# Kernel tuning notes

Measured on AMD Instinct MI355X. Metric: run time of the kernel, lower is better.

Reference implementation:

```python
import jax, jax.numpy as jnp
import numpy as np

B, K, S, H, V, T = 32, 5, 64, 768, 30522, 40
SEP = 102


def setup_inputs() -> dict:
    key = jax.random.key(0)
    ks = jax.random.split(key, 8)
    s = 0.02
    return {
        "src": jax.random.normal(ks[0], (B, S, H), jnp.float32),
        "E": jax.random.normal(ks[1], (V, H), jnp.float32) * s,
        "Wa": jax.random.normal(ks[2], (H, H), jnp.float32) * s,
        "Ua": jax.random.normal(ks[3], (H, H), jnp.float32) * s,
        "va": jax.random.normal(ks[4], (H,), jnp.float32) * s,
        "W_ih": jax.random.normal(ks[5], (3 * H, 2 * H), jnp.float32) * s,
        "W_hh": jax.random.normal(ks[6], (3 * H, H), jnp.float32) * s,
        "b_ih": jnp.zeros((3 * H,), jnp.float32),
        "b_hh": jnp.zeros((3 * H,), jnp.float32),
        "Wo": jax.random.normal(ks[7], (V, H), jnp.float32) * s,
        "bo": jnp.zeros((V,), jnp.float32),
    }


def _decoder(tok, src, h, E, Wa, Ua, va, W_ih, W_hh, b_ih, b_hh, Wo, bo):
    # tok [N] int, src [N,S,H], h [N,H] -> (logits [N,V], h_new [N,H])
    emb = E[tok]                                              # [N,H]
    e = jnp.tanh(src @ Wa + (h @ Ua)[:, None, :]) @ va        # [N,S]
    a = jax.nn.softmax(e, axis=-1)
    ctx = jnp.einsum('ns,nsd->nd', a, src)                    # [N,H]
    x = jnp.concatenate([emb, ctx], axis=-1)                  # [N,2H]
    gx = x @ W_ih.T + b_ih
    gh = h @ W_hh.T + b_hh
    xr, xz, xn = jnp.split(gx, 3, axis=-1)
    hr, hz, hn = jnp.split(gh, 3, axis=-1)
    r = jax.nn.sigmoid(xr + hr)
    z = jax.nn.sigmoid(xz + hz)
    n = jnp.tanh(xn + r * hn)
    h2 = (1.0 - z) * n + z * h
    return h2 @ Wo.T + bo, h2


def _search(src, E, Wa, Ua, va, W_ih, W_hh, b_ih, b_hh, Wo, bo):
    P = (E, Wa, Ua, va, W_ih, W_hh, b_ih, b_hh, Wo, bo)
    # step 0: start token 102, zero hidden
    tok0 = jnp.full((B,), SEP, jnp.int32)
    logits, h = _decoder(tok0, src, jnp.zeros((B, H), src.dtype), *P)
    logp = jax.nn.log_softmax(logits, axis=-1)
    scores, toks = jax.lax.top_k(logp, K)                     # [B,K]
    hiddens = jnp.broadcast_to(h[:, None, :], (B, K, H))
    src_k = jnp.broadcast_to(src[:, None], (B, K, S, H)).reshape(B * K, S, H)
    no_prob = jnp.full((V,), -1e9, src.dtype).at[SEP].set(0.0)
    beam_mask = jnp.arange(K) < K - 1  # original normalizes only first k-1 segments

    def body(carry, _):
        toks, maps, hiddens, scores, ended, lengths = carry
        # parent hidden per beam (gather by backpointer), decode all beams at once
        h_in = jnp.take_along_axis(hiddens, maps[:, :, None], axis=1)  # [B,K,H]
        logits, h_new = _decoder(toks.reshape(-1), src_k, h_in.reshape(B * K, H), *P)
        logp = jax.nn.log_softmax(logits, axis=-1).reshape(B, K, V)
        logp = jnp.where(ended[:, :, None] == 0, logp, no_prob)
        lengths = lengths + (ended == 0).astype(lengths.dtype)
        cand = logp + scores[:, :, None]                      # [B,K,V]
        denom = jnp.where(beam_mask, lengths ** 0.7, 1.0)     # [B,K]
        norm = (cand / denom[:, :, None]).reshape(B, K * V)
        _, idx = jax.lax.top_k(norm, K)                       # [B,K]
        new_scores = jnp.take_along_axis(cand.reshape(B, K * V), idx, axis=1)
        new_toks = (idx % V).astype(jnp.int32)
        new_maps = (idx // V).astype(jnp.int32)
        ended = jnp.where(new_toks == SEP, 1.0, ended)
        new_carry = (new_toks, new_maps, h_new.reshape(B, K, H), new_scores, ended, lengths)
        return new_carry, (new_toks, new_maps)

    carry0 = (toks.astype(jnp.int32), jnp.zeros((B, K), jnp.int32), hiddens,
              scores, jnp.zeros((B, K), src.dtype), jnp.zeros((B, K), src.dtype))
    carryF, (toks_seq, maps_seq) = jax.lax.scan(body, carry0, None, length=T - 1)
    toks_all = jnp.concatenate([toks[None].astype(jnp.int32), toks_seq], axis=0)   # [T,B,K]
    maps_all = jnp.concatenate([jnp.zeros((1, B, K), jnp.int32), maps_seq], axis=0)
    final_scores = carryF[3]
    best = jnp.argmax(final_scores, axis=1).astype(jnp.int32)  # [B]

    def back(idx, tm):
        tk, mp = tm
        out = jnp.take_along_axis(tk, idx[:, None], axis=1)[:, 0]
        nxt = jnp.take_along_axis(mp, idx[:, None], axis=1)[:, 0]
        return nxt, out

    _, outs = jax.lax.scan(back, best, (toks_all, maps_all), reverse=True)
    return outs.T, final_scores  # tokens [B,T], scores [B,K]


def reference(src, E, Wa, Ua, va, W_ih, W_hh, b_ih, b_hh, Wo, bo):
    tokens, _ = _search(src, E, Wa, Ua, va, W_ih, W_hh, b_ih, b_hh, Wo, bo)
    return tokens
```

## Files before the change

### kernel.cpp

```cpp
#include <hip/hip_runtime.h>
#include <cmath>

#define Hdim 768
#define Bb 32
#define Kb 5
#define Ss 64
#define Vv 30522
#define Tt 40
#define SEPTOK 102
#define NTLOG 477

typedef __attribute__((ext_vector_type(2))) float f32x2;
typedef __attribute__((ext_vector_type(4))) float f32x4;

struct Params {
    const float *src, *E, *Wa, *Ua, *va, *W_ih, *W_hh, *b_ih, *b_hh, *Wo, *bo;
    float *srcWa, *hA, *hB, *hUa, *gxE, *gh;
    float *mt_g; double *st_g; float *t5v; int *t5j;
    float *scores, *ended, *lengths;
    int *toks_cur, *maps_cur, *toks_all, *maps_all, *outTok;
};

__device__ __forceinline__ bool betterf(float va, int ja, float vb, int jb) {
    return (va > vb) || (va == vb && ja < jb);
}
__device__ __forceinline__ void ins5(float* tv, int* tj, float v, int j) {
    if (!betterf(v, j, tv[4], tj[4])) return;
    tv[4] = v; tj[4] = j;
#pragma unroll
    for (int q = 4; q > 0; q--) {
        if (betterf(tv[q], tj[q], tv[q - 1], tj[q - 1])) {
            float t = tv[q]; tv[q] = tv[q - 1]; tv[q - 1] = t;
            int  ti = tj[q]; tj[q] = tj[q - 1]; tj[q - 1] = ti;
        }
    }
}
__device__ __forceinline__ void ins5p(float* tv, int* tj, float* tx,
                                      float v, int j, float x) {
    if (!betterf(v, j, tv[4], tj[4])) return;
    tv[4] = v; tj[4] = j; tx[4] = x;
#pragma unroll
    for (int q = 4; q > 0; q--) {
        if (betterf(tv[q], tj[q], tv[q - 1], tj[q - 1])) {
            float t = tv[q]; tv[q] = tv[q - 1]; tv[q - 1] = t;
            int  ti = tj[q]; tj[q] = tj[q - 1]; tj[q - 1] = ti;
            float tz = tx[q]; tx[q] = tx[q - 1]; tx[q - 1] = tz;
        }
    }
}

struct GS { float xs[32][162]; float wt[32][68]; };

__device__ void gemm512(GS& sm, const Params& P, int t, int N, int xsrc,
    int i0, int Pdim, const float* __restrict__ W, int ldW, bool pmaj,
    const float* __restrict__ bias, float* __restrict__ outp, int ldO, int Icap)
{
    const int tid = threadIdx.x;
    const int ty = tid >> 5, tx = tid & 31;
    const float* h_old = (t & 1) ? P.hB : P.hA;

    float acc[10][2];
#pragma unroll
    for (int j = 0; j < 10; j++) { acc[j][0] = 0.f; acc[j][1] = 0.f; }

    for (int c0 = 0; c0 < Pdim; c0 += 32) {
        __syncthreads();
        for (int e = tid; e < 160 * 32; e += 512) {
            int r = e >> 5, p = e & 31;
            int n = (r < N) ? r : (N - 1);
            float v = 0.f;
            if (xsrc == 0) {
                if (t != 0) {
                    int par = (n / Kb) * Kb + P.maps_cur[n];
                    v = h_old[(size_t)par * Hdim + c0 + p];
                }
            } else {
                int tok = (t == 0) ? SEPTOK : P.toks_cur[n];
                v = P.E[(size_t)tok * Hdim + c0 + p];
            }
            sm.xs[p][r] = v;
        }
        if (pmaj) {
            int p = tid >> 4, i4 = (tid & 15) * 4;
            int gi = i0 + i4;
            f32x4 a;
            if (gi + 3 < Icap) {
                a = *(const f32x4*)&W[(size_t)(c0 + p) * ldW + gi];
            } else {
#pragma unroll
                for (int u = 0; u < 4; u++) {
                    int g = gi + u; if (g >= Icap) g = Icap - 1;
                    a[u] = W[(size_t)(c0 + p) * ldW + g];
                }
            }
            *(f32x4*)&sm.wt[p][i4] = a;
        } else {
            int c = tid >> 3, p4 = (tid & 7) * 4;
            int gi = i0 + c; if (gi >= Icap) gi = Icap - 1;
            f32x4 a = *(const f32x4*)&W[(size_t)gi * ldW + c0 + p4];
            sm.wt[p4 + 0][c] = a[0]; sm.wt[p4 + 1][c] = a[1];
            sm.wt[p4 + 2][c] = a[2]; sm.wt[p4 + 3][c] = a[3];
        }
        __syncthreads();
        float part[10][2];
#pragma unroll
        for (int j = 0; j < 10; j++) { part[j][0] = 0.f; part[j][1] = 0.f; }
#pragma unroll
        for (int p = 0; p < 32; p++) {
            f32x2 w2 = *(const f32x2*)&sm.wt[p][tx * 2];
            float xr[10];
#pragma unroll
            for (int j = 0; j < 10; j += 2) {
                f32x2 xv = *(const f32x2*)&sm.xs[p][ty * 10 + j];
                xr[j] = xv.x; xr[j + 1] = xv.y;
            }
#pragma unroll
            for (int j = 0; j < 10; j++) {
                part[j][0] = fmaf(xr[j], w2.x, part[j][0]);
                part[j][1] = fmaf(xr[j], w2.y, part[j][1]);
            }
        }
#pragma unroll
        for (int j = 0; j < 10; j++) {
            acc[j][0] = __fadd_rn(acc[j][0], part[j][0]);
            acc[j][1] = __fadd_rn(acc[j][1], part[j][1]);
        }
    }
#pragma unroll
    for (int j = 0; j < 10; j++) {
        int r = ty * 10 + j;
        if (r < N) {
#pragma unroll
            for (int u = 0; u < 2; u++) {
                int gi = i0 + tx * 2 + u;
                if (gi < Icap) {
                    float v = acc[j][u];
                    if (bias) v = __fadd_rn(v, bias[gi]);
                    outp[(size_t)r * ldO + gi] = v;
                }
            }
        }
    }
}

__global__ __launch_bounds__(512) void p1_k(Params P, int t, int N)
{
    __shared__ GS sm;
    int task = blockIdx.x;
    if (task < 12)
        gemm512(sm, P, t, N, 0, task * 64, Hdim, P.Ua, Hdim, true,
                nullptr, P.hUa, Hdim, Hdim);
    else if (task < 48)
        gemm512(sm, P, t, N, 0, (task - 12) * 64, Hdim, P.W_hh, Hdim, false,
                P.b_hh, P.gh, 2304, 2304);
    else
        gemm512(sm, P, t, N, 1, (task - 48) * 64, Hdim, P.W_ih, 1536, false,
                nullptr, P.gxE, 2304, 2304);
}

__global__ __launch_bounds__(512) void p2_k(Params P, int t, int N)
{
    __shared__ float hu[Hdim];
    __shared__ float va_s[Hdim];
    __shared__ float e_s[Ss];
    __shared__ float a_s[Ss];
    __shared__ float ctx[Hdim];
    __shared__ float gx[2304];
    const int tid = threadIdx.x;
    const int n = blockIdx.x;
    if (n >= N) return;
    const int Kcur = (t == 0) ? 1 : Kb;
    const int b = n / Kcur;
    float* h_new = (t & 1) ? P.hA : P.hB;
    const float* h_old = (t & 1) ? P.hB : P.hA;

    for (int j = tid; j < Hdim; j += 512) {
        hu[j]   = P.hUa[(size_t)n * Hdim + j];
        va_s[j] = P.va[j];
    }
    __syncthreads();
    {
        int wv = tid >> 6, ln = tid & 63;
        for (int s = wv * 8; s < wv * 8 + 8; s++) {
            const float* sw = P.srcWa + (size_t)(b * Ss + s) * Hdim;
            double p = 0.0;
            for (int j = ln; j < Hdim; j += 64) {
                float tv = tanhf(__fadd_rn(sw[j], hu[j]));
                p = ::fma((double)tv, (double)va_s[j], p);
            }
            for (int off = 32; off; off >>= 1) p += __shfl_down(p, off, 64);
            if (ln == 0) e_s[s] = (float)p;
        }
    }
    __syncthreads();
    if (tid < 64) {
        float v = e_s[tid], m = v;
        for (int off = 32; off; off >>= 1) m = fmaxf(m, __shfl_xor(m, off, 64));
        float p = expf(__fsub_rn(v, m));
        double sum = (double)p;
        for (int off = 32; off; off >>= 1) sum += __shfl_xor(sum, off, 64);
        a_s[tid] = __fdiv_rn(p, (float)sum);
    }
    __syncthreads();
    for (int j = tid; j < Hdim; j += 512) {
        double acc = 0.0;
        for (int s = 0; s < Ss; s++)
            acc = ::fma((double)a_s[s],
                        (double)P.src[(size_t)(b * Ss + s) * Hdim + j], acc);
        ctx[j] = (float)acc;
    }
    __syncthreads();
    for (int i = tid; i < 2304; i += 512) {
        const float* wr = P.W_ih + (size_t)i * 1536 + 768;
        float accv = 0.f, part = 0.f;
        for (int p = 0; p < 768; p += 4) {
            f32x4 w4 = *(const f32x4*)&wr[p];
            part = fmaf(ctx[p + 0], w4[0], part);
            part = fmaf(ctx[p + 1], w4[1], part);
            part = fmaf(ctx[p + 2], w4[2], part);
            part = fmaf(ctx[p + 3], w4[3], part);
            if ((p & 31) == 28) { accv = __fadd_rn(accv, part); part = 0.f; }
        }
        gx[i] = __fadd_rn(__fadd_rn(P.gxE[(size_t)n * 2304 + i], accv), P.b_ih[i]);
    }
    __syncthreads();
    int par = 0;
    if (t != 0) par = (n / Kb) * Kb + P.maps_cur[n];
    for (int i = tid; i < Hdim; i += 512) {
        float xr = gx[i], xz = gx[768 + i], xn = gx[1536 + i];
        const float* ghr = P.gh + (size_t)n * 2304;
        float hr = ghr[i], hz = ghr[768 + i], hn = ghr[1536 + i];
        float r  = __fdiv_rn(1.f, __fadd_rn(1.f, expf(-__fadd_rn(xr, hr))));
        float z  = __fdiv_rn(1.f, __fadd_rn(1.f, expf(-__fadd_rn(xz, hz))));
        float nn = tanhf(__fadd_rn(xn, __fmul_rn(r, hn)));
        float hv = (t == 0) ? 0.f : h_old[(size_t)par * Hdim + i];
        float h2 = __fadd_rn(__fmul_rn(__fsub_rn(1.f, z), nn), __fmul_rn(z, hv));
        if (t == 0) {
            for (int k = 0; k < Kb; k++)
                h_new[(size_t)(n * Kb + k) * Hdim + i] = h2;
        } else {
            h_new[(size_t)n * Hdim + i] = h2;
        }
    }
}

__global__ __launch_bounds__(512) void p4_k(Params P, int t, int N)
{
    __shared__ GS sm;
    const int tid = threadIdx.x;
    const int ty = tid >> 5, tx = tid & 31;
    const int task = blockIdx.x;
    const int i0 = task * 64;
    const float* h_new = (t & 1) ? P.hA : P.hB;
    const int rowMul = (t == 0) ? Kb : 1;

    float acc[10][2];
#pragma unroll
    for (int j = 0; j < 10; j++) { acc[j][0] = 0.f; acc[j][1] = 0.f; }

    for (int c0 = 0; c0 < Hdim; c0 += 32) {
        __syncthreads();
        for (int e = tid; e < 160 * 32; e += 512) {
            int r = e >> 5, p = e & 31;
            int n = (r < N) ? r : (N - 1);
            sm.xs[p][r] = h_new[((size_t)n * rowMul) * Hdim + c0 + p];
        }
        {
            int c = tid >> 3, p4 = (tid & 7) * 4;
            int gi = i0 + c; if (gi >= Vv) gi = Vv - 1;
            f32x4 a = *(const f32x4*)&P.Wo[(size_t)gi * Hdim + c0 + p4];
            sm.wt[p4 + 0][c] = a[0]; sm.wt[p4 + 1][c] = a[1];
            sm.wt[p4 + 2][c] = a[2]; sm.wt[p4 + 3][c] = a[3];
        }
        __syncthreads();
        float part[10][2];
#pragma unroll
        for (int j = 0; j < 10; j++) { part[j][0] = 0.f; part[j][1] = 0.f; }
#pragma unroll
        for (int p = 0; p < 32; p++) {
            f32x2 w2 = *(const f32x2*)&sm.wt[p][tx * 2];
            float xr[10];
#pragma unroll
            for (int j = 0; j < 10; j += 2) {
                f32x2 xv = *(const f32x2*)&sm.xs[p][ty * 10 + j];
                xr[j] = xv.x; xr[j + 1] = xv.y;
            }
#pragma unroll
            for (int j = 0; j < 10; j++) {
                part[j][0] = fmaf(xr[j], w2.x, part[j][0]);
                part[j][1] = fmaf(xr[j], w2.y, part[j][1]);
            }
        }
#pragma unroll
        for (int j = 0; j < 10; j++) {
            acc[j][0] = __fadd_rn(acc[j][0], part[j][0]);
            acc[j][1] = __fadd_rn(acc[j][1], part[j][1]);
        }
    }
#pragma unroll
    for (int j = 0; j < 10; j++) {
        int r = ty * 10 + j;
        int g0 = i0 + tx * 2, g1 = g0 + 1;
        float x0 = (g0 < Vv) ? __fadd_rn(acc[j][0], P.bo[g0]) : -INFINITY;
        float x1 = (g1 < Vv) ? __fadd_rn(acc[j][1], P.bo[g1]) : -INFINITY;
        float mr = fmaxf(x0, x1);
#pragma unroll
        for (int off = 16; off; off >>= 1)
            mr = fmaxf(mr, __shfl_xor(mr, off, 32));
        double s = (double)expf(__fsub_rn(x0, mr)) + (double)expf(__fsub_rn(x1, mr));
#pragma unroll
        for (int off = 16; off; off >>= 1)
            s += __shfl_xor(s, off, 32);
        float tv[5]; int tj[5];
#pragma unroll
        for (int q = 0; q < 5; q++) { tv[q] = -INFINITY; tj[q] = 0x7fffffff; }
        ins5(tv, tj, x0, (g0 < Vv) ? g0 : 0x7fffffff);
        ins5(tv, tj, x1, (g1 < Vv) ? g1 : 0x7fffffff);
#pragma unroll
        for (int lv = 1; lv < 32; lv <<= 1) {
            float pv[5]; int pj[5];
#pragma unroll
            for (int q = 0; q < 5; q++) {
                pv[q] = __shfl_xor(tv[q], lv, 32);
                pj[q] = __shfl_xor(tj[q], lv, 32);
            }
#pragma unroll
            for (int q = 0; q < 5; q++) ins5(tv, tj, pv[q], pj[q]);
        }
        if (tx == 0 && r < N) {
            P.mt_g[(size_t)task * 160 + r] = mr;
            P.st_g[(size_t)task * 160 + r] = s;
#pragma unroll
            for (int q = 0; q < 5; q++) {
                P.t5v[((size_t)task * 160 + r) * 5 + q] = tv[q];
                P.t5j[((size_t)task * 160 + r) * 5 + q] = tj[q];
            }
        }
    }
}

__global__ __launch_bounds__(512) void p5_k(Params P, int t)
{
    __shared__ float sc[Kb], den[Kb], endd[Kb], len[Kb], mxs[Kb], lgv[Kb];
    __shared__ float mv[256 * 5]; __shared__ int mj[256 * 5];
    __shared__ float mxp[256 * 5];
    __shared__ float rv[512]; __shared__ int rj[512]; __shared__ float rx[512];
    __shared__ double rd[512];
    __shared__ int selj[Kb]; __shared__ float selx[Kb];
    const int tid = threadIdx.x;
    const int b = blockIdx.x;
    const int Kcur = (t == 0) ? 1 : Kb;

    if (tid < Kb) {
        if (t == 0) {
            sc[tid] = 0.f; endd[tid] = 0.f; len[tid] = 0.f; den[tid] = 1.f;
        } else {
            float e0 = P.ended[b * Kb + tid];
            float ln = __fadd_rn(P.lengths[b * Kb + tid], (e0 == 0.f) ? 1.f : 0.f);
            sc[tid]  = P.scores[b * Kb + tid];
            endd[tid] = e0;
            len[tid] = ln;
            den[tid] = (tid < Kb - 1) ? (float)pow((double)ln, (double)0.7f) : 1.f;
        }
    }
    __syncthreads();
    for (int k = 0; k < Kcur; k++) {
        bool active = (t == 0) || (endd[k] == 0.f);
        if (!active) {
            if (tid == 0) { mxs[k] = 0.f; lgv[k] = 0.f; }
            __syncthreads();
            continue;
        }
        int n = b * Kcur + k;
        float m = -INFINITY;
        for (int tile = tid; tile < NTLOG; tile += 512)
            m = fmaxf(m, P.mt_g[(size_t)tile * 160 + n]);
        rv[tid] = m; __syncthreads();
        for (int off = 256; off; off >>= 1) {
            if (tid < off) rv[tid] = fmaxf(rv[tid], rv[tid + off]);
            __syncthreads();
        }
        m = rv[0];
        double s = 0.0;
        for (int tile = tid; tile < NTLOG; tile += 512)
            s += P.st_g[(size_t)tile * 160 + n] *
                 exp((double)(P.mt_g[(size_t)tile * 160 + n] - m));
        __syncthreads();
        rd[tid] = s; __syncthreads();
        for (int off = 256; off; off >>= 1) {
            if (tid < off) rd[tid] += rd[tid + off];
            __syncthreads();
        }
        if (tid == 0) {
            mxs[k] = m;
            float sf = (float)rd[0];
            lgv[k] = (float)log((double)sf);
        }
        __syncthreads();
    }
    float tv[5]; int tj[5]; float txx[5];
#pragma unroll
    for (int q = 0; q < 5; q++) { tv[q] = -INFINITY; tj[q] = 0x7fffffff; txx[q] = 0.f; }
    if (tid < 256) {
        int tot = Kcur * NTLOG * 5;
        for (int c = tid; c < tot; c += 256) {
            int k = c / (NTLOG * 5);
            if (t != 0 && endd[k] != 0.f) continue;
            int rm = c - k * NTLOG * 5;
            int tile = rm / 5, q = rm - tile * 5;
            int n = b * Kcur + k;
            int gi = P.t5j[((size_t)tile * 160 + n) * 5 + q];
            if (gi == 0x7fffffff) continue;
            float x = P.t5v[((size_t)tile * 160 + n) * 5 + q];
            float lp  = __fsub_rn(__fsub_rn(x, mxs[k]), lgv[k]);
            float val = __fdiv_rn(__fadd_rn(lp, sc[k]), den[k]);
            ins5p(tv, tj, txx, val, k * Vv + gi, x);
        }
    }
    if (tid == 0 && t != 0) {
        for (int k = 0; k < Kcur; k++)
            if (endd[k] != 0.f) {
                float val = __fdiv_rn(sc[k], den[k]);
                ins5p(tv, tj, txx, val, k * Vv + SEPTOK, 0.f);
            }
    }
    if (tid < 256) {
#pragma unroll
        for (int q = 0; q < 5; q++) {
            mv[tid * 5 + q] = tv[q];
            mj[tid * 5 + q] = tj[q];
            mxp[tid * 5 + q] = txx[q];
        }
    }
    __syncthreads();
    for (int pass = 0; pass < Kb; pass++) {
        if (tid < 256) {
            float bv = -INFINITY; int bj = 0x7fffffff; float bx = 0.f;
#pragma unroll
            for (int q = 0; q < 5; q++) {
                float v = mv[tid * 5 + q]; int j = mj[tid * 5 + q];
                if (betterf(v, j, bv, bj)) { bv = v; bj = j; bx = mxp[tid * 5 + q]; }
            }
            rv[tid] = bv; rj[tid] = bj; rx[tid] = bx;
        }
        __syncthreads();
        for (int off = 128; off; off >>= 1) {
            if (tid < off) {
                float ov = rv[tid + off]; int oj = rj[tid + off];
                if (betterf(ov, oj, rv[tid], rj[tid])) {
                    rv[tid] = ov; rj[tid] = oj; rx[tid] = rx[tid + off];
                }
            }
            __syncthreads();
        }
        if (tid == 0) { selj[pass] = rj[0]; selx[pass] = rx[0]; }
        __syncthreads();
        if (tid < 256) {
#pragma unroll
            for (int q = 0; q < 5; q++)
                if (mj[tid * 5 + q] == selj[pass]) {
                    mv[tid * 5 + q] = -INFINITY;
                    mj[tid * 5 + q] = 0x7fffffff;
                }
        }
        __syncthreads();
    }
    if (tid == 0) {
        for (int q = 0; q < Kb; q++) {
            int jj = selj[q];
            int pk = jj / Vv, vv = jj - pk * Vv;
            float lp;
            if (t == 0 || endd[pk] == 0.f)
                lp = __fsub_rn(__fsub_rn(selx[q], mxs[pk]), lgv[pk]);
            else
                lp = (vv == SEPTOK) ? 0.f : -1e9f;
            float cand = __fadd_rn(lp, sc[pk]);
            P.scores[b * Kb + q]   = cand;
            P.toks_cur[b * Kb + q] = vv;
            P.maps_cur[b * Kb + q] = (t == 0) ? 0 : pk;
            if (t == 0) {
                P.ended[b * Kb + q]   = 0.f;
                P.lengths[b * Kb + q] = 0.f;
            } else {
                P.ended[b * Kb + q]   = (vv == SEPTOK) ? 1.f : endd[q];
                P.lengths[b * Kb + q] = len[q];
            }
            P.toks_all[(size_t)t * Bb * Kb + b * Kb + q] = vv;
            P.maps_all[(size_t)t * Bb * Kb + b * Kb + q] = (t == 0) ? 0 : pk;
        }
    }
}

__global__ void back_k(Params P)
{
    int b = threadIdx.x;
    if (b >= Bb) return;
    int best = 0; float bvv = P.scores[b * Kb];
    for (int k = 1; k < Kb; k++) {
        float v = P.scores[b * Kb + k];
        if (v > bvv) { bvv = v; best = k; }
    }
    int cur = best;
    for (int t = Tt - 1; t >= 0; t--) {
        P.outTok[b * Tt + t] = P.toks_all[t * Bb * Kb + b * Kb + cur];
        cur = P.maps_all[t * Bb * Kb + b * Kb + cur];
    }
}

template<int RPT, int CPT, bool PMAJ>
__global__ __launch_bounds__(512) void gemmN_k(int P, int I, int xrs, int ldW,
    const float* __restrict__ X, const float* __restrict__ W,
    const float* __restrict__ bias, float* __restrict__ out, int ldO)
{
    constexpr int ROWS = RPT * 16;
    constexpr int COLS = CPT * 32;
    constexpr int XST  = ROWS + 4;
    constexpr int WST  = COLS + 4;
    __shared__ float xs[32][XST];
    __shared__ float wt[32][WST];
    const int tid = threadIdx.x;
    const int ty = tid >> 5, tx = tid & 31;
    const int row0 = blockIdx.y * ROWS;
    const int i0 = blockIdx.x * COLS;

    float acc[RPT][CPT];
#pragma unroll
    for (int j = 0; j < RPT; j++)
#pragma unroll
        for (int u = 0; u < CPT; u++) acc[j][u] = 0.f;

    for (int c0 = 0; c0 < P; c0 += 32) {
        __syncthreads();
        for (int e = tid; e < ROWS * 32; e += 512) {
            int r = e >> 5, p = e & 31;
            xs[p][r] = X[(size_t)(row0 + r) * xrs + c0 + p];
        }
        if (PMAJ) {
            for (int v = tid; v < 32 * (COLS / 4); v += 512) {
                int p  = v / (COLS / 4);
                int i4 = (v % (COLS / 4)) * 4;
                f32x4 a;
                if (i0 + i4 + 3 < I) {
                    a = *(const f32x4*)&W[(size_t)(c0 + p) * ldW + i0 + i4];
                } else {
#pragma unroll
                    for (int u = 0; u < 4; u++) {
                        int g = i0 + i4 + u; if (g >= I) g = I - 1;
                        a[u] = W[(size_t)(c0 + p) * ldW + g];
                    }
                }
                *(f32x4*)&wt[p][i4] = a;
            }
        } else {
            for (int v = tid; v < COLS * 8; v += 512) {
                int c  = v >> 3;
                int p4 = (v & 7) * 4;
                int gi = i0 + c; if (gi >= I) gi = I - 1;
                f32x4 a = *(const f32x4*)&W[(size_t)gi * ldW + c0 + p4];
                wt[p4 + 0][c] = a[0]; wt[p4 + 1][c] = a[1];
                wt[p4 + 2][c] = a[2]; wt[p4 + 3][c] = a[3];
            }
        }
        __syncthreads();
        float part[RPT][CPT];
#pragma unroll
        for (int j = 0; j < RPT; j++)
#pragma unroll
            for (int u = 0; u < CPT; u++) part[j][u] = 0.f;
#pragma unroll
        for (int p = 0; p < 32; p++) {
            float xr[RPT];
#pragma unroll
            for (int j = 0; j < RPT; j += 2) {
                f32x2 xv = *(const f32x2*)&xs[p][ty * RPT + j];
                xr[j] = xv.x; xr[j + 1] = xv.y;
            }
            float wv[CPT];
#pragma unroll
            for (int u = 0; u < CPT; u += 2) {
                f32x2 w2 = *(const f32x2*)&wt[p][tx * CPT + u];
                wv[u] = w2.x; wv[u + 1] = w2.y;
            }
#pragma unroll
            for (int j = 0; j < RPT; j++)
#pragma unroll
                for (int u = 0; u < CPT; u++)
                    part[j][u] = fmaf(xr[j], wv[u], part[j][u]);
        }
#pragma unroll
        for (int j = 0; j < RPT; j++)
#pragma unroll
            for (int u = 0; u < CPT; u++)
                acc[j][u] = __fadd_rn(acc[j][u], part[j][u]);
    }
#pragma unroll
    for (int j = 0; j < RPT; j++) {
        int gr = row0 + ty * RPT + j;
#pragma unroll
        for (int u = 0; u < CPT; u++) {
            int gi = i0 + tx * CPT + u;
            if (gi < I) {
                float v = acc[j][u];
                if (bias) v = __fadd_rn(v, bias[gi]);
                out[(size_t)gr * ldO + gi] = v;
            }
        }
    }
}

extern "C" void kernel_launch(void* const* d_in, const int* in_sizes, int n_in,
                              void* d_out, int out_size, void* d_ws, size_t ws_size,
                              hipStream_t stream)
{
    Params P;
    P.src  = (const float*)d_in[0];
    P.E    = (const float*)d_in[1];
    P.Wa   = (const float*)d_in[2];
    P.Ua   = (const float*)d_in[3];
    P.va   = (const float*)d_in[4];
    P.W_ih = (const float*)d_in[5];
    P.W_hh = (const float*)d_in[6];
    P.b_ih = (const float*)d_in[7];
    P.b_hh = (const float*)d_in[8];
    P.Wo   = (const float*)d_in[9];
    P.bo   = (const float*)d_in[10];
    P.outTok = (int*)d_out;

    char* w = (char*)d_ws;
    size_t used = 0;
    auto alloc = [&](size_t bytes) -> char* {
        char* p = w + used;
        used += (bytes + 255) & ~(size_t)255;
        return p;
    };
    P.srcWa   = (float*)alloc((size_t)Bb * Ss * Hdim * 4);
    P.hA      = (float*)alloc((size_t)Bb * Kb * Hdim * 4);
    P.hB      = (float*)alloc((size_t)Bb * Kb * Hdim * 4);
    P.hUa     = (float*)alloc((size_t)Bb * Kb * Hdim * 4);
    P.gxE     = (float*)alloc((size_t)Bb * Kb * 2304 * 4);
    P.gh      = (float*)alloc((size_t)Bb * Kb * 2304 * 4);
    P.mt_g    = (float*)alloc((size_t)NTLOG * 160 * 4);
    P.st_g    = (double*)alloc((size_t)NTLOG * 160 * 8);
    P.t5v     = (float*)alloc((size_t)NTLOG * 160 * 5 * 4);
    P.t5j     = (int*)alloc((size_t)NTLOG * 160 * 5 * 4);
    P.scores  = (float*)alloc(Bb * Kb * 4);
    P.ended   = (float*)alloc(Bb * Kb * 4);
    P.lengths = (float*)alloc(Bb * Kb * 4);
    P.toks_cur = (int*)alloc(Bb * Kb * 4);
    P.maps_cur = (int*)alloc(Bb * Kb * 4);
    P.toks_all = (int*)alloc((size_t)Tt * Bb * Kb * 4);
    P.maps_all = (int*)alloc((size_t)Tt * Bb * Kb * 4);

    gemmN_k<8, 2, true><<<dim3(12, 16), 512, 0, stream>>>(
        Hdim, Hdim, Hdim, Hdim, P.src, P.Wa, nullptr, P.srcWa, Hdim);

    for (int t = 0; t < Tt; t++) {
        int N = (t == 0) ? Bb : Bb * Kb;
        p1_k<<<84, 512, 0, stream>>>(P, t, N);
        p2_k<<<N, 512, 0, stream>>>(P, t, N);
        p4_k<<<NTLOG, 512, 0, stream>>>(P, t, N);
        p5_k<<<Bb, 512, 0, stream>>>(P, t);
    }
    back_k<<<1, 64, 0, stream>>>(P);
}
```

Measured before the change: 52.22 ms.

## Split attention-GRU kernel and batch context-to-gate projection as tiled GEMM

The fused per-row kernel that computed attention context, its W_ih projection and the GRU update is split into three kernels. The context projection now uses the shared tiled GEMM routine over all beam rows, so the weight slice is reused across rows instead of being streamed by every block. The gate update becomes a separate elementwise kernel. This adds two kernel launches per step and round-trips ctx and gx through global memory.

```diff
diff --git a/kernel.cpp b/kernel.cpp
--- a/kernel.cpp
+++ b/kernel.cpp
@@ -15,7 +15,7 @@
 
 struct Params {
     const float *src, *E, *Wa, *Ua, *va, *W_ih, *W_hh, *b_ih, *b_hh, *Wo, *bo;
-    float *srcWa, *hA, *hB, *hUa, *gxE, *gh;
+    float *srcWa, *hA, *hB, *hUa, *gxE, *gx, *gh, *ctx;
     float *mt_g; double *st_g; float *t5v; int *t5j;
     float *scores, *ended, *lengths;
     int *toks_cur, *maps_cur, *toks_all, *maps_all, *outTok;
@@ -53,7 +53,8 @@
 
 __device__ void gemm512(GS& sm, const Params& P, int t, int N, int xsrc,
     int i0, int Pdim, const float* __restrict__ W, int ldW, bool pmaj,
-    const float* __restrict__ bias, float* __restrict__ outp, int ldO, int Icap)
+    const float* __restrict__ bias, const float* __restrict__ addm, int ldA,
+    float* __restrict__ outp, int ldO, int Icap)
 {
     const int tid = threadIdx.x;
     const int ty = tid >> 5, tx = tid & 31;
@@ -74,9 +75,11 @@
                     int par = (n / Kb) * Kb + P.maps_cur[n];
                     v = h_old[(size_t)par * Hdim + c0 + p];
                 }
-            } else {
+            } else if (xsrc == 1) {
                 int tok = (t == 0) ? SEPTOK : P.toks_cur[n];
                 v = P.E[(size_t)tok * Hdim + c0 + p];
+            } else {
+                v = P.ctx[(size_t)n * Hdim + c0 + p];
             }
             sm.xs[p][r] = v;
         }
@@ -135,6 +138,7 @@
                 int gi = i0 + tx * 2 + u;
                 if (gi < Icap) {
                     float v = acc[j][u];
+                    if (addm) v = __fadd_rn(addm[(size_t)r * ldA + gi], v);
                     if (bias) v = __fadd_rn(v, bias[gi]);
                     outp[(size_t)r * ldO + gi] = v;
                 }
@@ -149,30 +153,26 @@
     int task = blockIdx.x;
     if (task < 12)
         gemm512(sm, P, t, N, 0, task * 64, Hdim, P.Ua, Hdim, true,
-                nullptr, P.hUa, Hdim, Hdim);
+                nullptr, nullptr, 0, P.hUa, Hdim, Hdim);
     else if (task < 48)
         gemm512(sm, P, t, N, 0, (task - 12) * 64, Hdim, P.W_hh, Hdim, false,
-                P.b_hh, P.gh, 2304, 2304);
+                P.b_hh, nullptr, 0, P.gh, 2304, 2304);
     else
         gemm512(sm, P, t, N, 1, (task - 48) * 64, Hdim, P.W_ih, 1536, false,
-                nullptr, P.gxE, 2304, 2304);
-}
-
-__global__ __launch_bounds__(512) void p2_k(Params P, int t, int N)
+                nullptr, nullptr, 0, P.gxE, 2304, 2304);
+}
+
+__global__ __launch_bounds__(512) void p2a_k(Params P, int t, int N)
 {
     __shared__ float hu[Hdim];
     __shared__ float va_s[Hdim];
     __shared__ float e_s[Ss];
     __shared__ float a_s[Ss];
-    __shared__ float ctx[Hdim];
-    __shared__ float gx[2304];
     const int tid = threadIdx.x;
     const int n = blockIdx.x;
     if (n >= N) return;
     const int Kcur = (t == 0) ? 1 : Kb;
     const int b = n / Kcur;
-    float* h_new = (t & 1) ? P.hA : P.hB;
-    const float* h_old = (t & 1) ? P.hB : P.hA;
 
     for (int j = tid; j < Hdim; j += 512) {
         hu[j]   = P.hUa[(size_t)n * Hdim + j];
@@ -207,40 +207,42 @@
         for (int s = 0; s < Ss; s++)
             acc = ::fma((double)a_s[s],
                         (double)P.src[(size_t)(b * Ss + s) * Hdim + j], acc);
-        ctx[j] = (float)acc;
-    }
-    __syncthreads();
-    for (int i = tid; i < 2304; i += 512) {
-        const float* wr = P.W_ih + (size_t)i * 1536 + 768;
-        float accv = 0.f, part = 0.f;
-        for (int p = 0; p < 768; p += 4) {
-            f32x4 w4 = *(const f32x4*)&wr[p];
-            part = fmaf(ctx[p + 0], w4[0], part);
-            part = fmaf(ctx[p + 1], w4[1], part);
-            part = fmaf(ctx[p + 2], w4[2], part);
-            part = fmaf(ctx[p + 3], w4[3], part);
-            if ((p & 31) == 28) { accv = __fadd_rn(accv, part); part = 0.f; }
-        }
-        gx[i] = __fadd_rn(__fadd_rn(P.gxE[(size_t)n * 2304 + i], accv), P.b_ih[i]);
-    }
-    __syncthreads();
-    int par = 0;
-    if (t != 0) par = (n / Kb) * Kb + P.maps_cur[n];
-    for (int i = tid; i < Hdim; i += 512) {
-        float xr = gx[i], xz = gx[768 + i], xn = gx[1536 + i];
-        const float* ghr = P.gh + (size_t)n * 2304;
-        float hr = ghr[i], hz = ghr[768 + i], hn = ghr[1536 + i];
-        float r  = __fdiv_rn(1.f, __fadd_rn(1.f, expf(-__fadd_rn(xr, hr))));
-        float z  = __fdiv_rn(1.f, __fadd_rn(1.f, expf(-__fadd_rn(xz, hz))));
-        float nn = tanhf(__fadd_rn(xn, __fmul_rn(r, hn)));
-        float hv = (t == 0) ? 0.f : h_old[(size_t)par * Hdim + i];
-        float h2 = __fadd_rn(__fmul_rn(__fsub_rn(1.f, z), nn), __fmul_rn(z, hv));
-        if (t == 0) {
-            for (int k = 0; k < Kb; k++)
-                h_new[(size_t)(n * Kb + k) * Hdim + i] = h2;
-        } else {
-            h_new[(size_t)n * Hdim + i] = h2;
-        }
+        P.ctx[(size_t)n * Hdim + j] = (float)acc;
+    }
+}
+
+__global__ __launch_bounds__(512) void p2b_k(Params P, int t, int N)
+{
+    __shared__ GS sm;
+    gemm512(sm, P, t, N, 2, blockIdx.x * 64, Hdim, P.W_ih + 768, 1536, false,
+            P.b_ih, P.gxE, 2304, P.gx, 2304, 2304);
+}
+
+__global__ __launch_bounds__(512) void p2c_k(Params P, int t, int N)
+{
+    int idx = blockIdx.x * 512 + threadIdx.x;
+    if (idx >= N * Hdim) return;
+    int n = idx / Hdim, i = idx - n * Hdim;
+    float* h_new = (t & 1) ? P.hA : P.hB;
+    const float* h_old = (t & 1) ? P.hB : P.hA;
+    const float* gxr = P.gx + (size_t)n * 2304;
+    const float* ghr = P.gh + (size_t)n * 2304;
+    float xr = gxr[i], xz = gxr[768 + i], xn = gxr[1536 + i];
+    float hr = ghr[i], hz = ghr[768 + i], hn = ghr[1536 + i];
+    float r  = __fdiv_rn(1.f, __fadd_rn(1.f, expf(-__fadd_rn(xr, hr))));
+    float z  = __fdiv_rn(1.f, __fadd_rn(1.f, expf(-__fadd_rn(xz, hz))));
+    float nn = tanhf(__fadd_rn(xn, __fmul_rn(r, hn)));
+    float hv = 0.f;
+    if (t != 0) {
+        int par = (n / Kb) * Kb + P.maps_cur[n];
+        hv = h_old[(size_t)par * Hdim + i];
+    }
+    float h2 = __fadd_rn(__fmul_rn(__fsub_rn(1.f, z), nn), __fmul_rn(z, hv));
+    if (t == 0) {
+        for (int k = 0; k < Kb; k++)
+            h_new[(size_t)(n * Kb + k) * Hdim + i] = h2;
+    } else {
+        h_new[(size_t)n * Hdim + i] = h2;
     }
 }
 
@@ -638,7 +640,9 @@
     P.hB      = (float*)alloc((size_t)Bb * Kb * Hdim * 4);
     P.hUa     = (float*)alloc((size_t)Bb * Kb * Hdim * 4);
     P.gxE     = (float*)alloc((size_t)Bb * Kb * 2304 * 4);
+    P.gx      = (float*)alloc((size_t)Bb * Kb * 2304 * 4);
     P.gh      = (float*)alloc((size_t)Bb * Kb * 2304 * 4);
+    P.ctx     = (float*)alloc((size_t)Bb * Kb * Hdim * 4);
     P.mt_g    = (float*)alloc((size_t)NTLOG * 160 * 4);
     P.st_g    = (double*)alloc((size_t)NTLOG * 160 * 8);
     P.t5v     = (float*)alloc((size_t)NTLOG * 160 * 5 * 4);
@@ -657,7 +661,9 @@
     for (int t = 0; t < Tt; t++) {
         int N = (t == 0) ? Bb : Bb * Kb;
         p1_k<<<84, 512, 0, stream>>>(P, t, N);
-        p2_k<<<N, 512, 0, stream>>>(P, t, N);
+        p2a_k<<<N, 512, 0, stream>>>(P, t, N);
+        p2b_k<<<36, 512, 0, stream>>>(P, t, N);
+        p2c_k<<<(N * Hdim + 511) / 512, 512, 0, stream>>>(P, t, N);
         p4_k<<<NTLOG, 512, 0, stream>>>(P, t, N);
         p5_k<<<Bb, 512, 0, stream>>>(P, t);
     }
```

Result: faster. 45.91 ms (-12.1%).
